# Kernel tuning notes

Measured on AMD Instinct MI355X. Metric: run time of the kernel, lower is better.

The kernel has to match this reference:

```python
import jax, jax.numpy as jnp
import numpy as np

EPS_NORM = 1e-7   # Normalize module eps (added to norm)
EPS_COS = 1e-8    # torch F.cosine_similarity default eps (clamped denom)


def _normalize(x):
    # Normalize(power=2): x / (||x||_2 + 1e-7), norm over dim 1
    n = jnp.sqrt(jnp.sum(x * x, axis=1, keepdims=True))
    return x / (n + EPS_NORM)


def _cos_sim_matrix(f):
    # pairwise cosine similarity, matching torch cosine_similarity semantics:
    # (f_i . f_j) / max(||f_i|| * ||f_j||, eps)
    n = jnp.linalg.norm(f, axis=1)            # [N]
    denom = jnp.maximum(n[:, None] * n[None, :], EPS_COS)
    return (f @ f.T) / denom                   # [N, N]


def setup_inputs() -> dict:
    key = jax.random.key(0)
    kq, kk = jax.random.split(key)
    N, D = 4096, 1024
    feat_q = jax.random.normal(kq, (N, D), dtype=jnp.float32)
    feat_k = jax.random.normal(kk, (N, D), dtype=jnp.float32)
    return {"feat_q": feat_q, "feat_k": feat_k}


def reference(feat_q, feat_k):
    q = _normalize(feat_q)
    k = jax.lax.stop_gradient(_normalize(feat_k))  # feat_k.detach()
    Sq = _cos_sim_matrix(q)   # [N, N]
    Sk = _cos_sim_matrix(k)   # [N, N]
    N = feat_q.shape[0]
    off_diag = ~jnp.eye(N, dtype=bool)
    diff2 = (Sq - Sk) ** 2
    # mean over the N*(N-1) off-diagonal (i != j) pairs
    loss = jnp.sum(jnp.where(off_diag, diff2, 0.0)) / (N * (N - 1))
    return loss
```

## Files before the change

### kernel.cpp

```cpp
#include <hip/hip_runtime.h>
#include <stdint.h>

#define N_ROWS 4096
#define DIMS   1024
#define TGR    16
#define NJOBT  72
#define KSPLIT 8
#define KCHUNK 512
#define BKB    128
#define NITER  4

typedef __attribute__((ext_vector_type(2))) long longx2;
typedef __attribute__((ext_vector_type(8))) unsigned short ushort8;
typedef __attribute__((ext_vector_type(4))) float f32x4;

__device__ __forceinline__ unsigned short f2bf(float f) {
  union { float f; unsigned int u; } c; c.f = f;
  unsigned int u = c.u;
  return (unsigned short)((u + 0x7fffu + ((u >> 16) & 1u)) >> 16);
}
__device__ __forceinline__ float bf2f(unsigned short v) {
  union { float f; unsigned int u; } c; c.u = ((unsigned int)v) << 16;
  return c.f;
}
__device__ __forceinline__ unsigned int pk4_fp8(float a, float b, float c, float d) {
  int v = __builtin_amdgcn_cvt_pk_fp8_f32(a, b, 0, false);
  v = __builtin_amdgcn_cvt_pk_fp8_f32(c, d, v, true);
  return (unsigned int)v;
}
__device__ __forceinline__ void async_cp16(const unsigned char* g, void* lds) {
  __builtin_amdgcn_global_load_lds(
      (const __attribute__((address_space(1))) void*)g,
      (__attribute__((address_space(3))) void*)lds, 16, 0, 0);
}

__global__ __launch_bounds__(256) void rownorm_kernel(
    const float* __restrict__ fq, const float* __restrict__ fk,
    float* __restrict__ invq, float* __restrict__ invk, float* __restrict__ out) {
  if (blockIdx.x == 0 && blockIdx.y == 0 && threadIdx.x == 0) out[0] = 0.0f;
  const int w = threadIdx.x >> 6, lane = threadIdx.x & 63;
  const int row = blockIdx.x * 4 + w;
  const float* src = blockIdx.y ? fk : fq;
  float* dst = blockIdx.y ? invk : invq;
  const float4* s4 = (const float4*)(src + (size_t)row * DIMS);
  float ss = 0.0f;
  #pragma unroll
  for (int s = 0; s < 4; ++s) {
    float4 v = s4[lane + 64 * s];
    ss += v.x * v.x + v.y * v.y + v.z * v.z + v.w * v.w;
  }
  #pragma unroll
  for (int off = 32; off > 0; off >>= 1) ss += __shfl_xor(ss, off);
  if (lane == 0) dst[row] = 1.0f / sqrtf(ss);
}

__global__ __launch_bounds__(256) void transpose_scale_kernel(
    const float* __restrict__ fq, const float* __restrict__ fk,
    const float* __restrict__ invq, const float* __restrict__ invk,
    unsigned char* __restrict__ Mt) {
  __shared__ unsigned short tile[64][260];
  const int i0 = blockIdx.x * 256;
  const int a0 = blockIdx.y * 64;
  const int w = threadIdx.x >> 6, lane = threadIdx.x & 63;
  const float* src;
  const float* inv;
  int acol;
  if (a0 < DIMS) { src = fq; inv = invq; acol = a0 + lane; }
  else           { src = fk; inv = invk; acol = a0 - DIMS + lane; }

  for (int c0 = 0; c0 < 64; c0 += 4) {
    ushort4 v;
    unsigned short* vp = (unsigned short*)&v;
    #pragma unroll
    for (int c = 0; c < 4; ++c) {
      const int i = i0 + w * 64 + c0 + c;
      vp[c] = f2bf(src[(size_t)i * DIMS + acol] * inv[i]);
    }
    *(ushort4*)&tile[lane][w * 64 + c0] = v;
  }
  __syncthreads();
  const int il = (lane * 4) & 127;
  const int blk = (i0 + lane * 4) >> 7;
  const int q = (il >> 3) & 3, s0b = (il >> 5) & 1, s1b = (il >> 6) & 1;
  const int pos = q * 32 + s1b * 16 + s0b * 8 + (il & 7);
  #pragma unroll
  for (int r = 0; r < 16; ++r) {
    const int al = w * 16 + r;
    ushort4 v = *(const ushort4*)&tile[al][lane * 4];
    const unsigned int p8 = pk4_fp8(bf2f(v.x), bf2f(v.y), bf2f(v.z), bf2f(v.w));
    *(unsigned int*)(Mt + (size_t)(a0 + al) * N_ROWS + blk * 128 + pos) = p8;
  }
}

__global__ __launch_bounds__(256, 2) void gram_grouped_kernel(
    const unsigned char* __restrict__ Mt, unsigned short* __restrict__ Gp) {
  __shared__ __align__(16) char smem[384 * 128];

  const int job = blockIdx.x;
  const int t = job >> 3;
  const int kc = job & 7;
  int R = 0, rem = t;
  while (rem >= 8 - (R >> 1)) { rem -= 8 - (R >> 1); ++R; }
  const int C = (R >> 1) + rem;
  const bool strad = ((R >> 1) == C);

  const int tid = threadIdx.x, w = tid >> 6, lane = tid & 63;
  const int rl = lane >> 3;
  const int cl = (lane & 7) ^ rl;

  const int ml = lane & 15, quad = lane >> 4;
  const int ar0 = (w >> 1) * 64, bc0 = (w & 1) * 128;
  const char* aBase = strad ? (smem + 16384 + (R & 1) * 16384) : smem;
  const char* bBase = smem + 16384;

  f32x4 acc[4][8] = {};

  for (int it = 0; it < NITER; ++it) {
    const size_t kof = (size_t)kc * KCHUNK + (size_t)it * BKB + cl * 16;
    if (!strad) {
      #pragma unroll
      for (int g = 0; g < 12; ++g) {
        const int rho = w * 96 + g * 8;
        const int grow = (rho < 128) ? (R * 128 + rho) : (C * 256 + rho - 128);
        async_cp16(Mt + (size_t)(grow + rl) * N_ROWS + kof,
                   smem + rho * 128 + lane * 16);
      }
    } else {
      #pragma unroll
      for (int g = 0; g < 8; ++g) {
        const int rho = 128 + w * 64 + g * 8;
        const int grow = C * 256 + rho - 128;
        async_cp16(Mt + (size_t)(grow + rl) * N_ROWS + kof,
                   smem + rho * 128 + lane * 16);
      }
    }
    __syncthreads();

    longx2 a[4][2], b[8][2];
    #pragma unroll
    for (int s1 = 0; s1 < 2; ++s1) {
      const int slot = ((quad * 2 + s1) ^ (ml & 7)) * 16;
      #pragma unroll
      for (int i = 0; i < 4; ++i)
        a[i][s1] = *(const longx2*)(aBase + (ar0 + i * 16 + ml) * 128 + slot);
      #pragma unroll
      for (int j = 0; j < 8; ++j)
        b[j][s1] = *(const longx2*)(bBase + (bc0 + j * 16 + ml) * 128 + slot);
    }
    #pragma unroll
    for (int s1 = 0; s1 < 2; ++s1)
      #pragma unroll
      for (int h = 0; h < 2; ++h)
        #pragma unroll
        for (int i = 0; i < 4; ++i)
          #pragma unroll
          for (int j = 0; j < 8; ++j)
            acc[i][j] = __builtin_amdgcn_mfma_f32_16x16x32_fp8_fp8(
                a[i][s1][h], b[j][s1][h], acc[i][j], 0, 0, 0);
    __syncthreads();
  }

  unsigned short* slab = Gp + (size_t)job * 32768 + w * 8192;
  #pragma unroll
  for (int i = 0; i < 4; ++i)
    #pragma unroll
    for (int j = 0; j < 8; ++j) {
      ushort4 o;
      o.x = f2bf(acc[i][j][0]); o.y = f2bf(acc[i][j][1]);
      o.z = f2bf(acc[i][j][2]); o.w = f2bf(acc[i][j][3]);
      *(ushort4*)(slab + (i * 8 + j) * 256 + lane * 4) = o;
    }
}

__global__ __launch_bounds__(256) void square_reduce_kernel(
    const unsigned short* __restrict__ Gp, float* __restrict__ out) {
  __shared__ float wsum[4];
  const int t = blockIdx.x >> 4;
  const int seg = blockIdx.x & 15;
  int R = 0, rem = t;
  while (rem >= 8 - (R >> 1)) { rem -= 8 - (R >> 1); ++R; }
  const int C = (R >> 1) + rem;
  const bool fullAbove = (R < 2 * C);

  const int off0 = seg * 2048 + threadIdx.x * 8;
  const unsigned short* base = Gp + (size_t)t * (KSPLIT * 32768) + off0;
  float s[8] = {0, 0, 0, 0, 0, 0, 0, 0};
  #pragma unroll
  for (int kc = 0; kc < KSPLIT; ++kc) {
    const ushort8 v = *(const ushort8*)(base + kc * 32768);
    #pragma unroll
    for (int x = 0; x < 8; ++x) s[x] += bf2f(v[x]);
  }

  float local = 0.0f;
  if (fullAbove) {
    #pragma unroll
    for (int x = 0; x < 8; ++x) local += 2.0f * s[x] * s[x];
  } else {
    #pragma unroll
    for (int x = 0; x < 8; ++x) {
      const int off = off0 + x;
      const int wv = off >> 13;
      const int rm = off & 8191;
      const int fi = rm >> 8;
      const int l4 = rm & 255;
      const int ln = l4 >> 2, p = l4 & 3;
      const int r = (wv >> 1) * 64 + (fi >> 3) * 16 + (ln >> 4) * 4 + p;
      const int c = (wv & 1) * 128 + (fi & 7) * 16 + (ln & 15);
      const int gr = R * 128 + r, gc = C * 256 + c;
      const float wgt = (gr < gc) ? 2.0f : (gr == gc ? 1.0f : 0.0f);
      local += wgt * s[x] * s[x];
    }
  }
  const float sgn = ((R < 8) == (C < 4)) ? 1.0f : -1.0f;
  local *= sgn;

  #pragma unroll
  for (int off = 32; off > 0; off >>= 1) local += __shfl_xor(local, off);
  const int w = threadIdx.x >> 6, lane = threadIdx.x & 63;
  if (lane == 0) wsum[w] = local;
  __syncthreads();
  if (threadIdx.x == 0) {
    const float ts = wsum[0] + wsum[1] + wsum[2] + wsum[3];
    atomicAdd(out, ts * (1.0f / 16773120.0f));
  }
}

extern "C" void kernel_launch(void* const* d_in, const int* in_sizes, int n_in,
                              void* d_out, int out_size, void* d_ws, size_t ws_size,
                              hipStream_t stream) {
  const float* fq = (const float*)d_in[0];
  const float* fk = (const float*)d_in[1];
  float* invq = (float*)d_ws;
  float* invk = invq + N_ROWS;
  unsigned char* Mt = (unsigned char*)d_ws + 32768;
  unsigned short* Gp = (unsigned short*)(Mt + (size_t)2048 * N_ROWS);
  float* out = (float*)d_out;

  rownorm_kernel<<<dim3(N_ROWS / 4, 2), 256, 0, stream>>>(fq, fk, invq, invk, out);
  transpose_scale_kernel<<<dim3(16, 32), 256, 0, stream>>>(fq, fk, invq, invk, Mt);
  gram_grouped_kernel<<<NJOBT * KSPLIT, 256, 0, stream>>>(Mt, Gp);
  square_reduce_kernel<<<NJOBT * 16, 256, 0, stream>>>(Gp, out);
}
```

Before: 134.0 us.

## Use 256x256 triangular Gram tiles with 512-thread blocks and double-buffered LDS

Replaces the 128x256 grouped Gram tiles (72 tiles, 256 threads) with square 256x256 upper-triangle tiles (36 tiles, 8 waves per block). The next K-slice is prefetched asynchronously into a second LDS buffer while the current one is consumed. B fragments are now loaded one column group at a time to reduce register pressure. The aim is more operand reuse per loaded byte and overlap of global-to-LDS traffic with MFMA work. The cost is 128KB of LDS per block, one block per CU, and 288 blocks that do not divide evenly across the CUs. The square-reduce kernel's indexing and diagonal masking are updated to match.

```diff
diff --git a/kernel.cpp b/kernel.cpp
--- a/kernel.cpp
+++ b/kernel.cpp
@@ -3,12 +3,14 @@
 
 #define N_ROWS 4096
 #define DIMS   1024
-#define TGR    16
-#define NJOBT  72
+#define BM 256
+#define TG 8
+#define NTRI 36
 #define KSPLIT 8
 #define KCHUNK 512
-#define BKB    128
-#define NITER  4
+#define BKB 128
+#define NITER 4
+#define NJOBS (NTRI * KSPLIT)
 
 typedef __attribute__((ext_vector_type(2))) long longx2;
 typedef __attribute__((ext_vector_type(8))) unsigned short ushort8;
@@ -92,75 +94,79 @@
   }
 }
 
-__global__ __launch_bounds__(256, 2) void gram_grouped_kernel(
+__global__ __launch_bounds__(512, 1) void gram_partial_kernel(
     const unsigned char* __restrict__ Mt, unsigned short* __restrict__ Gp) {
-  __shared__ __align__(16) char smem[384 * 128];
-
-  const int job = blockIdx.x;
-  const int t = job >> 3;
-  const int kc = job & 7;
-  int R = 0, rem = t;
-  while (rem >= 8 - (R >> 1)) { rem -= 8 - (R >> 1); ++R; }
-  const int C = (R >> 1) + rem;
-  const bool strad = ((R >> 1) == C);
+  __shared__ __align__(16) char smem[2][2 * BM * BKB];
+
+  const int t = blockIdx.x >> 3;
+  const int kc = blockIdx.x & 7;
+  int I = 0, rem = t;
+  while (rem >= (TG - I)) { rem -= (TG - I); ++I; }
+  const int J = I + rem;
 
   const int tid = threadIdx.x, w = tid >> 6, lane = tid & 63;
+
+  const int isB = w >> 2;
+  const int wq = w & 3;
+  const int rblk = isB ? J : I;
   const int rl = lane >> 3;
   const int cl = (lane & 7) ^ rl;
+  const bool skipStage = (isB && I == J);
+  const unsigned char* gsrc0 =
+      Mt + (size_t)(rblk * BM + wq * 64 + rl) * N_ROWS + kc * KCHUNK + cl * 16;
+  const int ldsOff = isB * 32768 + wq * 8192;
+  const int bOff = (I == J) ? 0 : 32768;
 
   const int ml = lane & 15, quad = lane >> 4;
   const int ar0 = (w >> 1) * 64, bc0 = (w & 1) * 128;
-  const char* aBase = strad ? (smem + 16384 + (R & 1) * 16384) : smem;
-  const char* bBase = smem + 16384;
 
   f32x4 acc[4][8] = {};
 
+  if (!skipStage) {
+    #pragma unroll
+    for (int s = 0; s < 8; ++s)
+      async_cp16(gsrc0 + (size_t)s * 8 * N_ROWS, smem[0] + ldsOff + s * 1024);
+  }
+
   for (int it = 0; it < NITER; ++it) {
-    const size_t kof = (size_t)kc * KCHUNK + (size_t)it * BKB + cl * 16;
-    if (!strad) {
-      #pragma unroll
-      for (int g = 0; g < 12; ++g) {
-        const int rho = w * 96 + g * 8;
-        const int grow = (rho < 128) ? (R * 128 + rho) : (C * 256 + rho - 128);
-        async_cp16(Mt + (size_t)(grow + rl) * N_ROWS + kof,
-                   smem + rho * 128 + lane * 16);
+    __syncthreads();
+    if (it + 1 < NITER && !skipStage) {
+      const unsigned char* g = gsrc0 + (it + 1) * BKB;
+      char* dst = smem[(it + 1) & 1] + ldsOff;
+      #pragma unroll
+      for (int s = 0; s < 8; ++s)
+        async_cp16(g + (size_t)s * 8 * N_ROWS, dst + s * 1024);
+    }
+    const char* buf = smem[it & 1];
+
+    longx2 a[4][2];
+    #pragma unroll
+    for (int i = 0; i < 4; ++i)
+      #pragma unroll
+      for (int s1 = 0; s1 < 2; ++s1) {
+        const int slot = ((quad * 2 + s1) ^ (ml & 7)) * 16;
+        a[i][s1] = *(const longx2*)(buf + (ar0 + i * 16 + ml) * BKB + slot);
       }
-    } else {
-      #pragma unroll
-      for (int g = 0; g < 8; ++g) {
-        const int rho = 128 + w * 64 + g * 8;
-        const int grow = C * 256 + rho - 128;
-        async_cp16(Mt + (size_t)(grow + rl) * N_ROWS + kof,
-                   smem + rho * 128 + lane * 16);
+    #pragma unroll
+    for (int j = 0; j < 8; ++j) {
+      longx2 b[2];
+      #pragma unroll
+      for (int s1 = 0; s1 < 2; ++s1) {
+        const int slot = ((quad * 2 + s1) ^ (ml & 7)) * 16;
+        b[s1] = *(const longx2*)(buf + bOff + (bc0 + j * 16 + ml) * BKB + slot);
       }
-    }
-    __syncthreads();
-
-    longx2 a[4][2], b[8][2];
-    #pragma unroll
-    for (int s1 = 0; s1 < 2; ++s1) {
-      const int slot = ((quad * 2 + s1) ^ (ml & 7)) * 16;
-      #pragma unroll
-      for (int i = 0; i < 4; ++i)
-        a[i][s1] = *(const longx2*)(aBase + (ar0 + i * 16 + ml) * 128 + slot);
-      #pragma unroll
-      for (int j = 0; j < 8; ++j)
-        b[j][s1] = *(const longx2*)(bBase + (bc0 + j * 16 + ml) * 128 + slot);
-    }
-    #pragma unroll
-    for (int s1 = 0; s1 < 2; ++s1)
-      #pragma unroll
-      for (int h = 0; h < 2; ++h)
+      #pragma unroll
+      for (int s1 = 0; s1 < 2; ++s1)
         #pragma unroll
-        for (int i = 0; i < 4; ++i)
+        for (int h = 0; h < 2; ++h)
           #pragma unroll
-          for (int j = 0; j < 8; ++j)
+          for (int i = 0; i < 4; ++i)
             acc[i][j] = __builtin_amdgcn_mfma_f32_16x16x32_fp8_fp8(
-                a[i][s1][h], b[j][s1][h], acc[i][j], 0, 0, 0);
-    __syncthreads();
-  }
-
-  unsigned short* slab = Gp + (size_t)job * 32768 + w * 8192;
+                a[i][s1][h], b[s1][h], acc[i][j], 0, 0, 0);
+    }
+  }
+
+  unsigned short* slab = Gp + (size_t)blockIdx.x * (BM * BM) + w * 8192;
   #pragma unroll
   for (int i = 0; i < 4; ++i)
     #pragma unroll
@@ -175,25 +181,24 @@
 __global__ __launch_bounds__(256) void square_reduce_kernel(
     const unsigned short* __restrict__ Gp, float* __restrict__ out) {
   __shared__ float wsum[4];
-  const int t = blockIdx.x >> 4;
-  const int seg = blockIdx.x & 15;
-  int R = 0, rem = t;
-  while (rem >= 8 - (R >> 1)) { rem -= 8 - (R >> 1); ++R; }
-  const int C = (R >> 1) + rem;
-  const bool fullAbove = (R < 2 * C);
+  const int t = blockIdx.x >> 5;
+  const int seg = blockIdx.x & 31;
+  int I = 0, rem = t;
+  while (rem >= (TG - I)) { rem -= (TG - I); ++I; }
+  const int J = I + rem;
 
   const int off0 = seg * 2048 + threadIdx.x * 8;
-  const unsigned short* base = Gp + (size_t)t * (KSPLIT * 32768) + off0;
+  const unsigned short* base = Gp + (size_t)t * (KSPLIT * BM * BM) + off0;
   float s[8] = {0, 0, 0, 0, 0, 0, 0, 0};
   #pragma unroll
   for (int kc = 0; kc < KSPLIT; ++kc) {
-    const ushort8 v = *(const ushort8*)(base + kc * 32768);
+    const ushort8 v = *(const ushort8*)(base + kc * (BM * BM));
     #pragma unroll
     for (int x = 0; x < 8; ++x) s[x] += bf2f(v[x]);
   }
 
   float local = 0.0f;
-  if (fullAbove) {
+  if (I != J) {
     #pragma unroll
     for (int x = 0; x < 8; ++x) local += 2.0f * s[x] * s[x];
   } else {
@@ -207,12 +212,11 @@
       const int ln = l4 >> 2, p = l4 & 3;
       const int r = (wv >> 1) * 64 + (fi >> 3) * 16 + (ln >> 4) * 4 + p;
       const int c = (wv & 1) * 128 + (fi & 7) * 16 + (ln & 15);
-      const int gr = R * 128 + r, gc = C * 256 + c;
-      const float wgt = (gr < gc) ? 2.0f : (gr == gc ? 1.0f : 0.0f);
+      const float wgt = (r < c) ? 2.0f : (r == c ? 1.0f : 0.0f);
       local += wgt * s[x] * s[x];
     }
   }
-  const float sgn = ((R < 8) == (C < 4)) ? 1.0f : -1.0f;
+  const float sgn = ((I < 4) == (J < 4)) ? 1.0f : -1.0f;
   local *= sgn;
 
   #pragma unroll
@@ -239,6 +243,6 @@
 
   rownorm_kernel<<<dim3(N_ROWS / 4, 2), 256, 0, stream>>>(fq, fk, invq, invk, out);
   transpose_scale_kernel<<<dim3(16, 32), 256, 0, stream>>>(fq, fk, invq, invk, Mt);
-  gram_grouped_kernel<<<NJOBT * KSPLIT, 256, 0, stream>>>(Mt, Gp);
-  square_reduce_kernel<<<NJOBT * 16, 256, 0, stream>>>(Gp, out);
-}
+  gram_partial_kernel<<<NJOBS, 512, 0, stream>>>(Mt, Gp);
+  square_reduce_kernel<<<NTRI * 32, 256, 0, stream>>>(Gp, out);
+}
```

Result: faster. 123.5 us (-7.9%).
